# Optimization experiments

Measured on AMD Instinct MI355X. Metric: run time of the kernel, lower is better.

Reference implementation:

```python
import jax, jax.numpy as jnp
import numpy as np

M, B, S, D, H = 3, 32, 256, 768, 1024
LN_EPS = 1e-5


def _ln(x, g, b):
    m = jnp.mean(x, axis=-1, keepdims=True)
    v = jnp.mean((x - m) ** 2, axis=-1, keepdims=True)
    return (x - m) / jnp.sqrt(v + LN_EPS) * g + b


def setup_inputs() -> dict:
    key = jax.random.key(0)
    ks = jax.random.split(key, 16)
    sc = 0.02  # weight init scale
    return {
        "feats": jax.random.normal(ks[0], (M, B, S, D), jnp.float32),
        "Wq": jax.random.normal(ks[1], (M, D, D), jnp.float32) * sc,
        "bq": jnp.zeros((M, D), jnp.float32),
        "Wk": jax.random.normal(ks[2], (M, D, D), jnp.float32) * sc,
        "bk": jnp.zeros((M, D), jnp.float32),
        "Wv": jax.random.normal(ks[3], (M, D, D), jnp.float32) * sc,
        "bv": jnp.zeros((M, D), jnp.float32),
        "pgq_w": jax.random.normal(ks[4], (M, D), jnp.float32) * sc,
        "pgq_b": jnp.zeros((M,), jnp.float32),
        "pgk_w": jax.random.normal(ks[5], (M, D), jnp.float32) * sc,
        "pgk_b": jnp.zeros((M,), jnp.float32),
        "mu_w": jax.random.normal(ks[6], (M, D), jnp.float32) * sc,
        "mu_b": jnp.zeros((M,), jnp.float32),
        "lv_w": jax.random.normal(ks[7], (M, D), jnp.float32) * sc,
        "lv_b": jnp.zeros((M,), jnp.float32),
        "dyn": jnp.ones((1,), jnp.float32),
        "WE_w": jax.random.normal(ks[8], (M, D, D), jnp.float32) * sc,
        "WE_b": jnp.zeros((M, D), jnp.float32),
        "Wh_w": jax.random.normal(ks[9], (M, D, D), jnp.float32) * sc,
        "Wh_b": jnp.zeros((M, D), jnp.float32),
        "Wqc_w": jax.random.normal(ks[10], (M, D, D), jnp.float32) * sc,
        "Wqc_b": jnp.zeros((M, D), jnp.float32),
        "lnE_g": jnp.ones((M, D), jnp.float32),
        "lnE_b": jnp.zeros((M, D), jnp.float32),
        "lnG_g": jnp.ones((M, D), jnp.float32),
        "lnG_b": jnp.zeros((M, D), jnp.float32),
        "out_w": jax.random.normal(ks[11], (D * M, H), jnp.float32) * sc,
        "out_b": jnp.zeros((H,), jnp.float32),
        "eps": jax.random.normal(ks[12], (M, M - 1, B, S, 1), jnp.float32),
    }


def reference(feats, Wq, bq, Wk, bk, Wv, bv, pgq_w, pgq_b, pgk_w, pgk_b,
              mu_w, mu_b, lv_w, lv_b, dyn, WE_w, WE_b, Wh_w, Wh_b, Wqc_w, Wqc_b,
              lnE_g, lnE_b, lnG_g, lnG_b, out_w, out_b, eps):
    # batched per-modality projections: [M,B,S,D]
    Qs = jnp.einsum('mbsd,mde->mbse', feats, Wq) + bq[:, None, None, :]
    Ks = jnp.einsum('mbsd,mde->mbse', feats, Wk) + bk[:, None, None, :]
    Vs = jnp.einsum('mbsd,mde->mbse', feats, Wv) + bv[:, None, None, :]
    scale = 1.0 / jnp.sqrt(jnp.float32(D))

    kl = jnp.float32(0.0)
    outs = []
    for i in range(M):
        Qi = Qs[i]  # [B,S,D]
        mu = jnp.einsum('bsd,d->bs', Qi, mu_w[i])[..., None] + mu_b[i]      # [B,S,1]
        lv = jnp.einsum('bsd,d->bs', Qi, lv_w[i])[..., None] + lv_b[i]      # [B,S,1]
        std = jnp.exp(0.5 * lv)
        pq_base = jax.nn.sigmoid(
            jnp.einsum('bsd,d->bs', Qi, pgq_w[i])[..., None] + pgq_b[i])    # [B,S,1]
        kl_i = -0.5 * jnp.sum(1.0 + lv - mu ** 2 - jnp.exp(lv))
        agg = jnp.zeros_like(Qi)
        cnt = 0
        for j in range(M):
            if j == i:
                continue
            d_gate = mu + dyn * std * eps[i, cnt]  # reparameterization
            cnt += 1
            kl = kl + kl_i
            g = jax.nn.sigmoid(d_gate)             # [B,S,1]
            p_q = pq_base * g
            p_k = jax.nn.sigmoid(
                jnp.einsum('bsd,d->bs', Ks[j], pgk_w[i])[..., None] + pgk_b[i]) * g
            A = jnp.einsum('bqd,bkd->bqk', Qi, Ks[j]) * scale
            A = A * p_q * jnp.swapaxes(p_k, 1, 2)  # pregated scores
            W = jax.nn.softmax(A, axis=-1)
            agg = agg + jnp.einsum('bqk,bkd->bqd', W, Vs[j])
        # CAG
        E = jax.nn.relu(agg @ WE_w[i] + WE_b[i])
        G = jax.nn.relu(agg @ Wh_w[i] + Wh_b[i] + Qi @ Wqc_w[i] + Wqc_b[i])
        Ci = _ln(E, lnE_g[i], lnE_b[i]) * _ln(G, lnG_g[i], lnG_b[i])
        outs.append(Ci)
    fused = jnp.concatenate(outs, axis=-1)[:, 0, :]  # [B, M*D]
    out = fused @ out_w + out_b                       # [B, H]
    return out, kl
```

## Files before the change

kernel.cpp:

```cpp
#include <hip/hip_runtime.h>

#define M 3
#define B 32
#define S 256
#define D 768
#define H 1024
#define MD (M * D)
#define NP (M * (M - 1))
#define SCALE 0.03608439182435161f
#define LN_EPS 1e-5f

#define OFF_WMU   0
#define OFF_WLV   2304
#define OFF_WPGQ  4608
#define OFF_WPK   6912
#define OFF_CMU   11520
#define OFF_CLV   11523
#define OFF_CPGQ  11526
#define OFF_CPK   11529
#define OFF_MU    11552
#define OFF_LV    36128
#define OFF_PKPRE 60704
#define OFF_PQPRE 109856
#define OFF_Q     109952
// ... 12 lines not shown
    #pragma unroll
    for (int o = 32; o > 0; o >>= 1) v += __shfl_down(v, o, 64);
    return v;
}

__device__ __forceinline__ float sigmoidf(float x) {
    return 1.0f / (1.0f + __expf(-x));
}

__device__ __forceinline__ float dot4(float4 a, float4 b) {
    return a.x * b.x + a.y * b.y + a.z * b.z + a.w * b.w;
}

__device__ __forceinline__ void fma4(float4& a, float s, float4 w) {
    a.x += s * w.x; a.y += s * w.y; a.z += s * w.z; a.w += s * w.w;
}

__global__ __launch_bounds__(256) void k_prep(const float* Wq, const float* Wk,
        const float* bq, const float* bk,
        const float* mu_w, const float* mu_b, const float* lv_w, const float* lv_b,
        const float* pgq_w, const float* pgq_b, const float* pgk_w, const float* pgk_b,
        float* ws) {
    int blk = blockIdx.x;
    if (blk < 72) {
        int mat = blk / 12, rg = blk % 12;
        const float* Wm; const float *va, *vb, *vc;
        float *oa, *ob, *oc; int nv;
        if (mat < 3) {
            int i = mat;
            Wm = Wq + i * D * D;
            va = mu_w + i * D; vb = lv_w + i * D; vc = pgq_w + i * D;
            oa = ws + OFF_WMU + i * D; ob = ws + OFF_WLV + i * D; oc = ws + OFF_WPGQ + i * D;
            nv = 3;
        } else {
            int j = mat - 3;
            int i1 = (j == 0) ? 1 : 0, i2 = (j == 2) ? 1 : 2;
            int p1 = 2 * i1 + ((j < i1) ? j : j - 1);
            int p2 = 2 * i2 + ((j < i2) ? j : j - 1);
            Wm = Wk + j * D * D;
            va = pgk_w + i1 * D; vb = pgk_w + i2 * D; vc = va;
            oa = ws + OFF_WPK + p1 * D; ob = ws + OFF_WPK + p2 * D; oc = oa;
            nv = 2;
        }
        int wave = threadIdx.x >> 6, lane = threadIdx.x & 63;
        const float4* va4 = (const float4*)va;
        const float4* vb4 = (const float4*)vb;
// ... 39 lines not shown
        __shared__ float r[4];
        if ((t & 63) == 0) r[t >> 6] = part;
        __syncthreads();
        if (t == 0) *out = r[0] + r[1] + r[2] + r[3] + bias;
    } else {
        int r = blk - 87;
        int j = r / 144; r = r % 144;
        int d0 = (r / 12) * 64, e0 = (r % 12) * 64;
        __shared__ float tile[64][65];
        const float* src = Wk + j * D * D;
        for (int idx = threadIdx.x; idx < 4096; idx += 256) {
            int rr = idx / 64, cc = idx % 64;
            tile[rr][cc] = src[(d0 + rr) * D + e0 + cc];
        }
        __syncthreads();
        float* dst = ws + OFF_WKT + j * D * D;
        for (int idx = threadIdx.x; idx < 4096; idx += 256) {
            int rr = idx / 64, cc = idx % 64;
            dst[(e0 + rr) * D + d0 + cc] = tile[cc][rr];
        }
    }
}

__global__ __launch_bounds__(256) void k_stats(const float* feats, float* ws) {
    __shared__ float klred[4];
    int wave = threadIdx.x >> 6, lane = threadIdx.x & 63;
    int m = blockIdx.x / 512;
    int row0 = blockIdx.x * 16 + wave * 4;
    int i1 = (m == 0) ? 1 : 0, i2 = (m == 2) ? 1 : 2;
    int p0 = 2 * i1 + ((m < i1) ? m : m - 1);
    int p1 = 2 * i2 + ((m < i2) ? m : m - 1);
    const float4* wmu  = (const float4*)(ws + OFF_WMU + m * D);
    const float4* wlv  = (const float4*)(ws + OFF_WLV + m * D);
    const float4* wpgq = (const float4*)(ws + OFF_WPGQ + m * D);
    const float4* wpk0 = (const float4*)(ws + OFF_WPK + p0 * D);
    const float4* wpk1 = (const float4*)(ws + OFF_WPK + p1 * D);
    float4 U0 = wmu[lane],  U1 = wmu[lane + 64],  U2 = wmu[lane + 128];
    float4 L0 = wlv[lane],  L1 = wlv[lane + 64],  L2 = wlv[lane + 128];
    float4 Q0 = wpgq[lane], Q1 = wpgq[lane + 64], Q2 = wpgq[lane + 128];
    float4 P0 = wpk0[lane], P1 = wpk0[lane + 64], P2 = wpk0[lane + 128];
    float4 R0 = wpk1[lane], R1 = wpk1[lane + 64], R2 = wpk1[lane + 128];
    float4 x[4][3];
    #pragma unroll
    for (int rr = 0; rr < 4; rr++) {
        const float4* f = (const float4*)(feats + (size_t)(row0 + rr) * D);
        x[rr][0] = f[lane]; x[rr][1] = f[lane + 64]; x[rr][2] = f[lane + 128];
    }
    float amu[4], alv[4], apgq[4], apk0[4], apk1[4];
    #pragma unroll
    for (int rr = 0; rr < 4; rr++) {
        amu[rr]  = dot4(x[rr][0], U0) + dot4(x[rr][1], U1) + dot4(x[rr][2], U2);
        alv[rr]  = dot4(x[rr][0], L0) + dot4(x[rr][1], L1) + dot4(x[rr][2], L2);
        apgq[rr] = dot4(x[rr][0], Q0) + dot4(x[rr][1], Q1) + dot4(x[rr][2], Q2);
        apk0[rr] = dot4(x[rr][0], P0) + dot4(x[rr][1], P1) + dot4(x[rr][2], P2);
        apk1[rr] = dot4(x[rr][0], R0) + dot4(x[rr][1], R1) + dot4(x[rr][2], R2);
    }
    #pragma unroll
    for (int rr = 0; rr < 4; rr++) {
        amu[rr] = wave_reduce(amu[rr]);  alv[rr] = wave_reduce(alv[rr]);
        apgq[rr] = wave_reduce(apgq[rr]);
        apk0[rr] = wave_reduce(apk0[rr]); apk1[rr] = wave_reduce(apk1[rr]);
    }
    if (lane == 0) {
        float cmu = ws[OFF_CMU + m], clv = ws[OFF_CLV + m];
        float cpgq = ws[OFF_CPGQ + m];
        float cpk0 = ws[OFF_CPK + p0], cpk1 = ws[OFF_CPK + p1];
        float klsum = 0.f;
        #pragma unroll
        for (int rr = 0; rr < 4; rr++) {
            int row = row0 + rr;
            int rem = row % (B * S);
            int b = rem / S, s = rem % S;
            float muv = amu[rr] + cmu;
            float lvv = alv[rr] + clv;
            ws[OFF_MU + row] = muv;
            ws[OFF_LV + row] = lvv;
            ws[OFF_PKPRE + (p0 * B + b) * S + s] = apk0[rr] + cpk0;
            ws[OFF_PKPRE + (p1 * B + b) * S + s] = apk1[rr] + cpk1;
            if (s == 0) ws[OFF_PQPRE + m * B + b] = apgq[rr] + cpgq;
            klsum += 1.0f + lvv - muv * muv - __expf(lvv);
        }
        klred[wave] = klsum;
    }
    __syncthreads();
    if (threadIdx.x == 0)
        atomicAdd(ws + OFF_KL, -(klred[0] + klred[1] + klred[2] + klred[3]));
}


__global__ __launch_bounds__(192) void k_qrow(const float* feats, const float* Wq, float* ws) {
    int blk = blockIdx.x;
    int i = blk / 96, r = blk % 96, bg = r / 24, kc = r % 24;
    int kbase = kc * 32;
    __shared__ __align__(16) float xs[32][8];
    for (int idx = threadIdx.x; idx < 256; idx += 192) {
        int d = idx / 8, bb = idx % 8;
        xs[d][bb] = feats[((size_t)(i * B + bg * 8 + bb) * S) * D + kbase + d];
    }
    __syncthreads();
    int e4 = threadIdx.x * 4;
    const float* Wm = Wq + i * D * D + kbase * D + e4;
    float4 acc[8];
    #pragma unroll
    for (int bb = 0; bb < 8; bb++) acc[bb] = make_float4(0.f, 0.f, 0.f, 0.f);
    for (int k = 0; k < 32; k++) {
        float4 w = *(const float4*)(Wm + k * D);
        float4 x0 = *(const float4*)&xs[k][0];
        float4 x1 = *(const float4*)&xs[k][4];
        fma4(acc[0], x0.x, w); fma4(acc[1], x0.y, w);
        fma4(acc[2], x0.z, w); fma4(acc[3], x0.w, w);
        fma4(acc[4], x1.x, w); fma4(acc[5], x1.y, w);
        fma4(acc[6], x1.z, w); fma4(acc[7], x1.w, w);
    }
    #pragma unroll
    for (int bb = 0; bb < 8; bb++)
        *(float4*)&ws[OFF_ARENA + kc * 73728 + (i * 32 + bg * 8 + bb) * 768 + e4] = acc[bb];
}

__global__ __launch_bounds__(256) void k_red_q(const float* bq, const float* bk, float* ws) {
    int blk = blockIdx.x;
    int i = blk / B, b = blk % B;
    int fbase = (i * B + b) * D;
    int t = threadIdx.x;
    __shared__ float4 qsh[192];
    __shared__ float redsh[8];
    if (t < 192) {
        float4 a = *(const float4*)&bq[i * D + t * 4];
        #pragma unroll
        for (int kc = 0; kc < 24; kc++) {
            float4 v = *(const float4*)&ws[OFF_ARENA + kc * 73728 + fbase + t * 4];
            a.x += v.x; a.y += v.y; a.z += v.z; a.w += v.w;
        }
        *(float4*)&ws[OFF_Q + fbase + t * 4] = a;
        qsh[t] = a;
    }
    __syncthreads();
    int jA = (i == 0) ? 1 : 0, jB = (i == 2) ? 1 : 2;
    float pA_ = 0.f, pB_ = 0.f;
    if (t < 192) {
        float4 q = qsh[t];
        pA_ = dot4(q, *(const float4*)&bk[jA * D + t * 4]);
        pB_ = dot4(q, *(const float4*)&bk[jB * D + t * 4]);
    }
    pA_ = wave_reduce(pA_); pB_ = wave_reduce(pB_);
    int wave = t >> 6, lane = t & 63;
    if (lane == 0) { redsh[wave] = pA_; redsh[4 + wave] = pB_; }
    __syncthreads();
    if (t == 0) {
        ws[OFF_QBK + (2 * i) * B + b]     = redsh[0] + redsh[1] + redsh[2] + redsh[3];
        ws[OFF_QBK + (2 * i + 1) * B + b] = redsh[4] + redsh[5] + redsh[6] + redsh[7];
    }
}

__global__ __launch_bounds__(192) void k_qk(float* ws) {
    int blk = blockIdx.x;
    int j = blk / 96, r = blk % 96, vg = r / 12, kc = r % 12;
    int kbase = kc * 64;
    int i1 = (j == 0) ? 1 : 0, i2 = (j == 2) ? 1 : 2;
    __shared__ __align__(16) float xs[64][8];
    for (int idx = threadIdx.x; idx < 512; idx += 192) {
        int d = idx / 8, v = idx % 8;
        int v64 = vg * 8 + v;
        int i_ = (v64 < 32) ? i1 : i2, b = v64 & 31;
        xs[d][v] = ws[OFF_Q + (i_ * 32 + b) * 768 + kbase + d];
    }
    __syncthreads();
    int e4 = threadIdx.x * 4;
    const float* Wm = ws + OFF_WKT + j * D * D + kbase * D + e4;
    float4 acc[8];
    #pragma unroll
    for (int bb = 0; bb < 8; bb++) acc[bb] = make_float4(0.f, 0.f, 0.f, 0.f);
    for (int k = 0; k < 64; k++) {
        float4 w = *(const float4*)(Wm + k * D);
        float4 x0 = *(const float4*)&xs[k][0];
        float4 x1 = *(const float4*)&xs[k][4];
        fma4(acc[0], x0.x, w); fma4(acc[1], x0.y, w);
        fma4(acc[2], x0.z, w); fma4(acc[3], x0.w, w);
        fma4(acc[4], x1.x, w); fma4(acc[5], x1.y, w);
        fma4(acc[6], x1.z, w); fma4(acc[7], x1.w, w);
    }
    #pragma unroll
    for (int v = 0; v < 8; v++)
        *(float4*)&ws[OFF_ARENA + kc * 147456 + (j * 64 + vg * 8 + v) * 768 + e4] = acc[v];
}

__global__ __launch_bounds__(256) void k_red_qk(float* ws) {
    int idx = blockIdx.x * 256 + threadIdx.x;
    int fidx = idx * 4;
    int p = fidx / 24576, rem = fidx % 24576;
    int b = rem / 768, d = rem % 768;
    int i = p / 2, c = p % 2, j = c + (c >= i ? 1 : 0);
    int i1 = (j == 0) ? 1 : 0;
    int iidx = (i == i1) ? 0 : 1;
    int vg = iidx * 32 + b;
    float4 a = make_float4(0.f, 0.f, 0.f, 0.f);
    #pragma unroll
    for (int kc = 0; kc < 12; kc++) {
        float4 pp = *(const float4*)&ws[OFF_ARENA + kc * 147456 + (j * 64 + vg) * 768 + d];
        a.x += pp.x; a.y += pp.y; a.z += pp.z; a.w += pp.w;
    }
    *(float4*)&ws[OFF_QK + fidx] = a;
}

__global__ __launch_bounds__(256) void k_score(const float* feats, float* ws) {
    int blk = blockIdx.x;
    int j = blk / 128, r = blk % 128, b = r / 4, kc = r % 4;
    int i1 = (j == 0) ? 1 : 0, i2 = (j == 2) ? 1 : 2;
    int pA = 2 * i1 + ((j < i1) ? j : j - 1);
    int pB = 2 * i2 + ((j < i2) ? j : j - 1);
    int wave = threadIdx.x >> 6, lane = threadIdx.x & 63;
    const float4* qa4 = (const float4*)(ws + OFF_QK + (pA * B + b) * D);
    const float4* qb4 = (const float4*)(ws + OFF_QK + (pB * B + b) * D);
    float4 qA0 = qa4[lane], qA1 = qa4[lane + 64], qA2 = qa4[lane + 128];
    float4 qB0 = qb4[lane], qB1 = qb4[lane + 64], qB2 = qb4[lane + 128];
    const float* fbase = feats + ((j * B + b) * S) * D;
    float* scA = ws + OFF_ARENA + ((j * B + b) * 2) * S;
    float* scB = scA + S;
    int k0 = kc * 64 + wave * 16;
    for (int k = k0; k < k0 + 16; k += 4) {
        float4 x[4][3];
        #pragma unroll
        for (int rr = 0; rr < 4; rr++) {
            const float4* f = (const float4*)(fbase + (k + rr) * D);
            x[rr][0] = f[lane]; x[rr][1] = f[lane + 64]; x[rr][2] = f[lane + 128];
        }
        float dA[4], dB[4];
        #pragma unroll
        for (int rr = 0; rr < 4; rr++) {
            dA[rr] = dot4(x[rr][0], qA0) + dot4(x[rr][1], qA1) + dot4(x[rr][2], qA2);
            dB[rr] = dot4(x[rr][0], qB0) + dot4(x[rr][1], qB1) + dot4(x[rr][2], qB2);
        }
        #pragma unroll
        for (int rr = 0; rr < 4; rr++) { dA[rr] = wave_reduce(dA[rr]); dB[rr] = wave_reduce(dB[rr]); }
        if (lane == 0) {
            #pragma unroll
            for (int rr = 0; rr < 4; rr++) { scA[k + rr] = dA[rr]; scB[k + rr] = dB[rr]; }
        }
    }
}

__global__ __launch_bounds__(256) void k_wsum(const float* feats, const float* eps,
                                              const float* dyn, float* ws) {
    int blk = blockIdx.x;
    int j = blk / 96, r = blk % 96, b = r / 3, dc = r % 3;
    int i1 = (j == 0) ? 1 : 0, i2 = (j == 2) ? 1 : 2;
    int pA = 2 * i1 + ((j < i1) ? j : j - 1);
    int pB = 2 * i2 + ((j < i2) ? j : j - 1);
    __shared__ float sA[S], sB[S], redm[256];
    int t = threadIdx.x;
    float dynv = dyn[0];
    const float* rawA = ws + OFF_ARENA + ((j * B + b) * 2) * S;
    const float* rawB = rawA + S;
    {
        float muk = ws[OFF_MU + (i1 * B + b) * S + t];
        float lvk = ws[OFF_LV + (i1 * B + b) * S + t];
        float ek  = eps[(pA * B + b) * S + t];
        float g   = sigmoidf(muk + dynv * __expf(0.5f * lvk) * ek);
        float pk  = sigmoidf(ws[OFF_PKPRE + (pA * B + b) * S + t]) * g;
        float mu0 = ws[OFF_MU + (i1 * B + b) * S];
        float lv0 = ws[OFF_LV + (i1 * B + b) * S];
        float e0  = eps[(pA * B + b) * S];
// ... 28 lines not shown
    for (int st = 128; st > 0; st >>= 1) { if (t < st) redm[t] = fmaxf(redm[t], redm[t + st]); __syncthreads(); }
    float mxB = redm[0]; __syncthreads();
    float wB = __expf(sB[t] - mxB);
    redm[t] = wB; __syncthreads();
    for (int st = 128; st > 0; st >>= 1) { if (t < st) redm[t] += redm[t + st]; __syncthreads(); }
    float sumB = redm[0]; __syncthreads();
    sB[t] = wB / sumB;
    __syncthreads();
    int dim = dc * 256 + t;
    const float* fcol = feats + ((j * B + b) * S) * D + dim;
    float accA = 0.f, accB = 0.f;
    #pragma unroll 8
    for (int k = 0; k < S; k++) {
        float fv = fcol[k * D];
        accA += sA[k] * fv;
        accB += sB[k] * fv;
    }
    ws[OFF_FSUM + (pA * B + b) * D + dim] = accA;
    ws[OFF_FSUM + (pB * B + b) * D + dim] = accB;
}

__global__ __launch_bounds__(192) void k_agg(const float* Wv, float* ws) {
    int blk = blockIdx.x;
    int i = blk / 96, r = blk % 96, bg = r / 24, kc = r % 24;
    int kbase = kc * 32;
    int j0 = (i == 0) ? 1 : 0, j1 = (i == 2) ? 1 : 2;
    int p0 = 2 * i, p1 = 2 * i + 1;
    __shared__ __align__(16) float xs0[32][8], xs1[32][8];
    for (int idx = threadIdx.x; idx < 256; idx += 192) {
        int d = idx / 8, bb = idx % 8;
        xs0[d][bb] = ws[OFF_FSUM + (p0 * B + bg * 8 + bb) * D + kbase + d];
        xs1[d][bb] = ws[OFF_FSUM + (p1 * B + bg * 8 + bb) * D + kbase + d];
    }
    __syncthreads();
    int e4 = threadIdx.x * 4;
    const float* W0 = Wv + j0 * D * D + kbase * D + e4;
    const float* W1 = Wv + j1 * D * D + kbase * D + e4;
    float4 acc[8];
    #pragma unroll
    for (int bb = 0; bb < 8; bb++) acc[bb] = make_float4(0.f, 0.f, 0.f, 0.f);
    for (int k = 0; k < 32; k++) {
        float4 w0 = *(const float4*)(W0 + k * D);
        float4 w1 = *(const float4*)(W1 + k * D);
        float4 a0 = *(const float4*)&xs0[k][0];
        float4 a1 = *(const float4*)&xs0[k][4];
        float4 b0 = *(const float4*)&xs1[k][0];
        float4 b1 = *(const float4*)&xs1[k][4];
        fma4(acc[0], a0.x, w0); fma4(acc[1], a0.y, w0);
        fma4(acc[2], a0.z, w0); fma4(acc[3], a0.w, w0);
        fma4(acc[4], a1.x, w0); fma4(acc[5], a1.y, w0);
        fma4(acc[6], a1.z, w0); fma4(acc[7], a1.w, w0);
        fma4(acc[0], b0.x, w1); fma4(acc[1], b0.y, w1);
        fma4(acc[2], b0.z, w1); fma4(acc[3], b0.w, w1);
        fma4(acc[4], b1.x, w1); fma4(acc[5], b1.y, w1);
        fma4(acc[6], b1.z, w1); fma4(acc[7], b1.w, w1);
    }
    #pragma unroll
    for (int bb = 0; bb < 8; bb++)
        *(float4*)&ws[OFF_ARENA + kc * 73728 + (i * 32 + bg * 8 + bb) * 768 + e4] = acc[bb];
}

__global__ __launch_bounds__(256) void k_red_agg(const float* bv, float* ws) {
    int idx = blockIdx.x * 256 + threadIdx.x;
    int fidx = idx * 4;
    int i = fidx / 24576, e = fidx % 768;
    int j0 = (i == 0) ? 1 : 0, j1 = (i == 2) ? 1 : 2;
    float4 b0 = *(const float4*)&bv[j0 * 768 + e];
    float4 b1 = *(const float4*)&bv[j1 * 768 + e];
    float4 a = make_float4(b0.x + b1.x, b0.y + b1.y, b0.z + b1.z, b0.w + b1.w);
    const float* base = ws + OFF_ARENA;
    #pragma unroll
    for (int kc = 0; kc < 24; kc++) {
        float4 p = *(const float4*)&base[kc * 73728 + fidx];
        a.x += p.x; a.y += p.y; a.z += p.z; a.w += p.w;
    }
    *(float4*)&ws[OFF_AGG + fidx] = a;
}

__global__ __launch_bounds__(192) void k_eg(const float* WE_w, const float* Wh_w,
                                            const float* Wqc_w, float* ws) {
    int blk = blockIdx.x;
    int kind = blk / 144, r = blk % 144;
    int i = r / 48, r2 = r % 48, bg = r2 / 12, kc = r2 % 12;
    int kbase = kc * 64;
    __shared__ __align__(16) float xa[64][8], xq[64][8];
    for (int idx = threadIdx.x; idx < 512; idx += 192) {
        int d = idx / 8, bb = idx % 8;
        xa[d][bb] = ws[OFF_AGG + (i * B + bg * 8 + bb) * D + kbase + d];
        if (kind) xq[d][bb] = ws[OFF_Q + (i * B + bg * 8 + bb) * D + kbase + d];
    }
    __syncthreads();
    int e4 = threadIdx.x * 4;
    float4 acc[8];
    #pragma unroll
    for (int bb = 0; bb < 8; bb++) acc[bb] = make_float4(0.f, 0.f, 0.f, 0.f);
    if (kind == 0) {
        const float* Wm = WE_w + i * D * D + kbase * D + e4;
        for (int k = 0; k < 64; k++) {
            float4 w = *(const float4*)(Wm + k * D);
            float4 a0 = *(const float4*)&xa[k][0];
            float4 a1 = *(const float4*)&xa[k][4];
            fma4(acc[0], a0.x, w); fma4(acc[1], a0.y, w);
            fma4(acc[2], a0.z, w); fma4(acc[3], a0.w, w);
            fma4(acc[4], a1.x, w); fma4(acc[5], a1.y, w);
            fma4(acc[6], a1.z, w); fma4(acc[7], a1.w, w);
        }
    } else {
        const float* Wh = Wh_w + i * D * D + kbase * D + e4;
        const float* Wc = Wqc_w + i * D * D + kbase * D + e4;
        for (int k = 0; k < 64; k++) {
            float4 wh = *(const float4*)(Wh + k * D);
            float4 wc = *(const float4*)(Wc + k * D);
            float4 a0 = *(const float4*)&xa[k][0];
            float4 a1 = *(const float4*)&xa[k][4];
            float4 q0 = *(const float4*)&xq[k][0];
            float4 q1 = *(const float4*)&xq[k][4];
            fma4(acc[0], a0.x, wh); fma4(acc[1], a0.y, wh);
            fma4(acc[2], a0.z, wh); fma4(acc[3], a0.w, wh);
            fma4(acc[4], a1.x, wh); fma4(acc[5], a1.y, wh);
            fma4(acc[6], a1.z, wh); fma4(acc[7], a1.w, wh);
            fma4(acc[0], q0.x, wc); fma4(acc[1], q0.y, wc);
            fma4(acc[2], q0.z, wc); fma4(acc[3], q0.w, wc);
            fma4(acc[4], q1.x, wc); fma4(acc[5], q1.y, wc);
            fma4(acc[6], q1.z, wc); fma4(acc[7], q1.w, wc);
        }
    }
    int base = OFF_ARENA + (kind ? 884736 : 0) + kc * 73728;
    #pragma unroll
    for (int bb = 0; bb < 8; bb++)
        *(float4*)&ws[base + (i * 32 + bg * 8 + bb) * 768 + e4] = acc[bb];
}

__global__ __launch_bounds__(256) void k_red_eg(const float* WE_b, const float* Wh_b,
                                                const float* Wqc_b, float* ws) {
    int blk = blockIdx.x;
    bool isG = blk >= 72;
    int idx = (isG ? blk - 72 : blk) * 256 + threadIdx.x;
    int fidx = idx * 4;
    int i = fidx / 24576, e = fidx % 768;
    float4 a;
    const float* base = ws + OFF_ARENA + (isG ? 884736 : 0);
    if (isG) {
        float4 b0 = *(const float4*)&Wh_b[i * 768 + e];
        float4 b1 = *(const float4*)&Wqc_b[i * 768 + e];
        a = make_float4(b0.x + b1.x, b0.y + b1.y, b0.z + b1.z, b0.w + b1.w);
    } else {
        a = *(const float4*)&WE_b[i * 768 + e];
    }
    #pragma unroll
    for (int kc = 0; kc < 12; kc++) {
        float4 p = *(const float4*)&base[kc * 73728 + fidx];
        a.x += p.x; a.y += p.y; a.z += p.z; a.w += p.w;
    }
// ... 15 lines not shown
    r2[t] = e0 * e0 + e1 * e1 + e2 * e2;
    r3[t] = g0 + g1 + g2;
    r4[t] = g0 * g0 + g1 * g1 + g2 * g2;
    __syncthreads();
    for (int st = 128; st > 0; st >>= 1) {
        if (t < st) { r1[t] += r1[t + st]; r2[t] += r2[t + st]; r3[t] += r3[t + st]; r4[t] += r4[t + st]; }
        __syncthreads();
    }
    float mE = r1[0] * (1.0f / D), vE = r2[0] * (1.0f / D) - mE * mE;
    float mG = r3[0] * (1.0f / D), vG = r4[0] * (1.0f / D) - mG * mG;
    float sE = rsqrtf(vE + LN_EPS), sG = rsqrtf(vG + LN_EPS);
    float* o = ws + OFF_FUSED + b * MD + i * D;
    const float* eg = lnE_g + i * D; const float* ebv = lnE_b + i * D;
    const float* gg = lnG_g + i * D; const float* gbv = lnG_b + i * D;
    o[t]       = ((e0 - mE) * sE * eg[t]       + ebv[t])       * ((g0 - mG) * sG * gg[t]       + gbv[t]);
    o[t + 256] = ((e1 - mE) * sE * eg[t + 256] + ebv[t + 256]) * ((g1 - mG) * sG * gg[t + 256] + gbv[t + 256]);
    o[t + 512] = ((e2 - mE) * sE * eg[t + 512] + ebv[t + 512]) * ((g2 - mG) * sG * gg[t + 512] + gbv[t + 512]);
}

__global__ __launch_bounds__(256) void k_out(const float* out_w, float* ws) {
    int blk = blockIdx.x;
    int bg = blk / 36, kc = blk % 36;
    int kbase = kc * 64;
    __shared__ __align__(16) float xs[64][8];
    for (int idx = threadIdx.x; idx < 512; idx += 256) {
        int d = idx / 8, bb = idx % 8;
        xs[d][bb] = ws[OFF_FUSED + (bg * 8 + bb) * MD + kbase + d];
    }
    __syncthreads();
    int e4 = threadIdx.x * 4;
    const float* Wm = out_w + kbase * H + e4;
    float4 acc[8];
    #pragma unroll
    for (int bb = 0; bb < 8; bb++) acc[bb] = make_float4(0.f, 0.f, 0.f, 0.f);
    for (int k = 0; k < 64; k++) {
        float4 w = *(const float4*)(Wm + k * H);
        float4 x0 = *(const float4*)&xs[k][0];
        float4 x1 = *(const float4*)&xs[k][4];
        fma4(acc[0], x0.x, w); fma4(acc[1], x0.y, w);
        fma4(acc[2], x0.z, w); fma4(acc[3], x0.w, w);
        fma4(acc[4], x1.x, w); fma4(acc[5], x1.y, w);
        fma4(acc[6], x1.z, w); fma4(acc[7], x1.w, w);
    }
    #pragma unroll
    for (int bb = 0; bb < 8; bb++)
        *(float4*)&ws[OFF_ARENA + kc * 32768 + (bg * 8 + bb) * 1024 + e4] = acc[bb];
}

__global__ __launch_bounds__(256) void k_fin(const float* out_b, float* ws, float* out) {
    int b = blockIdx.x;
    int h4 = threadIdx.x * 4;
    float4 a = *(const float4*)&out_b[h4];
    #pragma unroll
    for (int kc = 0; kc < 36; kc++) {
        float4 p = *(const float4*)&ws[OFF_ARENA + kc * 32768 + b * 1024 + h4];
        a.x += p.x; a.y += p.y; a.z += p.z; a.w += p.w;
    }
    *(float4*)&out[b * H + h4] = a;
    if (b == 0 && threadIdx.x == 0) out[B * H] = ws[OFF_KL];
}

extern "C" void kernel_launch(void* const* d_in, const int* in_sizes, int n_in,
                              void* d_out, int out_size, void* d_ws, size_t ws_size,
                              hipStream_t stream) {
    const float* feats = (const float*)d_in[0];
    const float* Wq    = (const float*)d_in[1];
    const float* bq    = (const float*)d_in[2];
    const float* Wk    = (const float*)d_in[3];
    const float* bk    = (const float*)d_in[4];
// ... 4 lines not shown
    const float* pgk_w = (const float*)d_in[9];
    const float* pgk_b = (const float*)d_in[10];
    const float* mu_w  = (const float*)d_in[11];
    const float* mu_b  = (const float*)d_in[12];
    const float* lv_w  = (const float*)d_in[13];
    const float* lv_b  = (const float*)d_in[14];
    const float* dyn   = (const float*)d_in[15];
    const float* WE_w  = (const float*)d_in[16];
    const float* WE_b  = (const float*)d_in[17];
    const float* Wh_w  = (const float*)d_in[18];
    const float* Wh_b  = (const float*)d_in[19];
    const float* Wqc_w = (const float*)d_in[20];
    const float* Wqc_b = (const float*)d_in[21];
    const float* lnE_g = (const float*)d_in[22];
    const float* lnE_b = (const float*)d_in[23];
    const float* lnG_g = (const float*)d_in[24];
    const float* lnG_b = (const float*)d_in[25];
    const float* out_w = (const float*)d_in[26];
    const float* out_b = (const float*)d_in[27];
    const float* eps   = (const float*)d_in[28];
    float* ws  = (float*)d_ws;
    float* out = (float*)d_out;

    hipMemsetAsync((char*)d_ws + OFF_KL * sizeof(float), 0, sizeof(float), stream);

    k_prep<<<519, 256, 0, stream>>>(Wq, Wk, bq, bk, mu_w, mu_b, lv_w, lv_b,
                                    pgq_w, pgq_b, pgk_w, pgk_b, ws);
    k_stats<<<1536, 256, 0, stream>>>(feats, ws);
    k_qrow<<<288, 192, 0, stream>>>(feats, Wq, ws);
    k_red_q<<<96, 256, 0, stream>>>(bq, bk, ws);
    k_qk<<<288, 192, 0, stream>>>(ws);
    k_red_qk<<<144, 256, 0, stream>>>(ws);
    k_score<<<384, 256, 0, stream>>>(feats, ws);
    k_wsum<<<288, 256, 0, stream>>>(feats, eps, dyn, ws);
    k_agg<<<288, 192, 0, stream>>>(Wv, ws);
    k_red_agg<<<72, 256, 0, stream>>>(bv, ws);
    k_eg<<<288, 192, 0, stream>>>(WE_w, Wh_w, Wqc_w, ws);
    k_red_eg<<<144, 256, 0, stream>>>(WE_b, Wh_b, Wqc_b, ws);
    k_ln<<<M * B, 256, 0, stream>>>(lnE_g, lnE_b, lnG_g, lnG_b, ws);
    k_out<<<144, 256, 0, stream>>>(out_w, ws);
    k_fin<<<32, 256, 0, stream>>>(out_b, ws, out);
}
```

Measured before the change: 360.9 us.

## Fuse per-row gate statistics into score kernel and widen batch tiles to 16

Removes the separate k_stats pass over all of feats by computing the mu, logvar and p_k projections, the KL partial sums and the pq prelogit inside k_score, which already streams the same feature rows. The KL accumulator is now zeroed inside k_prep, replacing the separate memset. The skinny GEMM kernels (qrow, qk, agg, eg, out) now process 16 batch rows per block instead of 8, halving grid sizes and doubling weight reuse per load. The trade-off is more registers per thread and fewer blocks, which may leave CUs idle. k_score also now issues many more wave reductions per row.

After: 417.1 us. 15.6% more time.

```diff
diff --git a/kernel.cpp b/kernel.cpp
--- a/kernel.cpp
+++ b/kernel.cpp
@@ -58,6 +58,7 @@
         const float* pgq_w, const float* pgq_b, const float* pgk_w, const float* pgk_b,
         float* ws) {
     int blk = blockIdx.x;
+    if (blk == 0 && threadIdx.x == 0) ws[OFF_KL] = 0.f;
     if (blk < 72) {
         int mat = blk / 12, rg = blk % 12;
         const float* Wm; const float *va, *vb, *vc;
@@ -143,99 +144,39 @@
     }
 }
 
-__global__ __launch_bounds__(256) void k_stats(const float* feats, float* ws) {
-    __shared__ float klred[4];
-    int wave = threadIdx.x >> 6, lane = threadIdx.x & 63;
-    int m = blockIdx.x / 512;
-    int row0 = blockIdx.x * 16 + wave * 4;
-    int i1 = (m == 0) ? 1 : 0, i2 = (m == 2) ? 1 : 2;
-    int p0 = 2 * i1 + ((m < i1) ? m : m - 1);
-    int p1 = 2 * i2 + ((m < i2) ? m : m - 1);
-    const float4* wmu  = (const float4*)(ws + OFF_WMU + m * D);
-    const float4* wlv  = (const float4*)(ws + OFF_WLV + m * D);
-    const float4* wpgq = (const float4*)(ws + OFF_WPGQ + m * D);
-    const float4* wpk0 = (const float4*)(ws + OFF_WPK + p0 * D);
-    const float4* wpk1 = (const float4*)(ws + OFF_WPK + p1 * D);
-    float4 U0 = wmu[lane],  U1 = wmu[lane + 64],  U2 = wmu[lane + 128];
-    float4 L0 = wlv[lane],  L1 = wlv[lane + 64],  L2 = wlv[lane + 128];
-    float4 Q0 = wpgq[lane], Q1 = wpgq[lane + 64], Q2 = wpgq[lane + 128];
-    float4 P0 = wpk0[lane], P1 = wpk0[lane + 64], P2 = wpk0[lane + 128];
-    float4 R0 = wpk1[lane], R1 = wpk1[lane + 64], R2 = wpk1[lane + 128];
-    float4 x[4][3];
-    #pragma unroll
-    for (int rr = 0; rr < 4; rr++) {
-        const float4* f = (const float4*)(feats + (size_t)(row0 + rr) * D);
-        x[rr][0] = f[lane]; x[rr][1] = f[lane + 64]; x[rr][2] = f[lane + 128];
-    }
-    float amu[4], alv[4], apgq[4], apk0[4], apk1[4];
-    #pragma unroll
-    for (int rr = 0; rr < 4; rr++) {
-        amu[rr]  = dot4(x[rr][0], U0) + dot4(x[rr][1], U1) + dot4(x[rr][2], U2);
-        alv[rr]  = dot4(x[rr][0], L0) + dot4(x[rr][1], L1) + dot4(x[rr][2], L2);
-        apgq[rr] = dot4(x[rr][0], Q0) + dot4(x[rr][1], Q1) + dot4(x[rr][2], Q2);
-        apk0[rr] = dot4(x[rr][0], P0) + dot4(x[rr][1], P1) + dot4(x[rr][2], P2);
-        apk1[rr] = dot4(x[rr][0], R0) + dot4(x[rr][1], R1) + dot4(x[rr][2], R2);
-    }
-    #pragma unroll
-    for (int rr = 0; rr < 4; rr++) {
-        amu[rr] = wave_reduce(amu[rr]);  alv[rr] = wave_reduce(alv[rr]);
-        apgq[rr] = wave_reduce(apgq[rr]);
-        apk0[rr] = wave_reduce(apk0[rr]); apk1[rr] = wave_reduce(apk1[rr]);
-    }
-    if (lane == 0) {
-        float cmu = ws[OFF_CMU + m], clv = ws[OFF_CLV + m];
-        float cpgq = ws[OFF_CPGQ + m];
-        float cpk0 = ws[OFF_CPK + p0], cpk1 = ws[OFF_CPK + p1];
-        float klsum = 0.f;
-        #pragma unroll
-        for (int rr = 0; rr < 4; rr++) {
-            int row = row0 + rr;
-            int rem = row % (B * S);
-            int b = rem / S, s = rem % S;
-            float muv = amu[rr] + cmu;
-            float lvv = alv[rr] + clv;
-            ws[OFF_MU + row] = muv;
-            ws[OFF_LV + row] = lvv;
-            ws[OFF_PKPRE + (p0 * B + b) * S + s] = apk0[rr] + cpk0;
-            ws[OFF_PKPRE + (p1 * B + b) * S + s] = apk1[rr] + cpk1;
-            if (s == 0) ws[OFF_PQPRE + m * B + b] = apgq[rr] + cpgq;
-            klsum += 1.0f + lvv - muv * muv - __expf(lvv);
-        }
-        klred[wave] = klsum;
-    }
-    __syncthreads();
-    if (threadIdx.x == 0)
-        atomicAdd(ws + OFF_KL, -(klred[0] + klred[1] + klred[2] + klred[3]));
-}
-
-
 __global__ __launch_bounds__(192) void k_qrow(const float* feats, const float* Wq, float* ws) {
     int blk = blockIdx.x;
-    int i = blk / 96, r = blk % 96, bg = r / 24, kc = r % 24;
+    int i = blk / 48, r = blk % 48, bg = r / 24, kc = r % 24;
     int kbase = kc * 32;
-    __shared__ __align__(16) float xs[32][8];
-    for (int idx = threadIdx.x; idx < 256; idx += 192) {
-        int d = idx / 8, bb = idx % 8;
-        xs[d][bb] = feats[((size_t)(i * B + bg * 8 + bb) * S) * D + kbase + d];
+    __shared__ __align__(16) float xs[32][16];
+    for (int idx = threadIdx.x; idx < 512; idx += 192) {
+        int d = idx / 16, bb = idx % 16;
+        xs[d][bb] = feats[((size_t)(i * B + bg * 16 + bb) * S) * D + kbase + d];
     }
     __syncthreads();
     int e4 = threadIdx.x * 4;
     const float* Wm = Wq + i * D * D + kbase * D + e4;
-    float4 acc[8];
-    #pragma unroll
-    for (int bb = 0; bb < 8; bb++) acc[bb] = make_float4(0.f, 0.f, 0.f, 0.f);
+    float4 acc[16];
+    #pragma unroll
+    for (int bb = 0; bb < 16; bb++) acc[bb] = make_float4(0.f, 0.f, 0.f, 0.f);
     for (int k = 0; k < 32; k++) {
         float4 w = *(const float4*)(Wm + k * D);
         float4 x0 = *(const float4*)&xs[k][0];
         float4 x1 = *(const float4*)&xs[k][4];
-        fma4(acc[0], x0.x, w); fma4(acc[1], x0.y, w);
-        fma4(acc[2], x0.z, w); fma4(acc[3], x0.w, w);
-        fma4(acc[4], x1.x, w); fma4(acc[5], x1.y, w);
-        fma4(acc[6], x1.z, w); fma4(acc[7], x1.w, w);
-    }
-    #pragma unroll
-    for (int bb = 0; bb < 8; bb++)
-        *(float4*)&ws[OFF_ARENA + kc * 73728 + (i * 32 + bg * 8 + bb) * 768 + e4] = acc[bb];
+        float4 x2 = *(const float4*)&xs[k][8];
+        float4 x3 = *(const float4*)&xs[k][12];
+        fma4(acc[0], x0.x, w);  fma4(acc[1], x0.y, w);
+        fma4(acc[2], x0.z, w);  fma4(acc[3], x0.w, w);
+        fma4(acc[4], x1.x, w);  fma4(acc[5], x1.y, w);
+        fma4(acc[6], x1.z, w);  fma4(acc[7], x1.w, w);
+        fma4(acc[8], x2.x, w);  fma4(acc[9], x2.y, w);
+        fma4(acc[10], x2.z, w); fma4(acc[11], x2.w, w);
+        fma4(acc[12], x3.x, w); fma4(acc[13], x3.y, w);
+        fma4(acc[14], x3.z, w); fma4(acc[15], x3.w, w);
+    }
+    #pragma unroll
+    for (int bb = 0; bb < 16; bb++)
+        *(float4*)&ws[OFF_ARENA + kc * 73728 + (i * 32 + bg * 16 + bb) * 768 + e4] = acc[bb];
 }
 
 __global__ __launch_bounds__(256) void k_red_q(const float* bq, const float* bk, float* ws) {
@@ -275,34 +216,40 @@
 
 __global__ __launch_bounds__(192) void k_qk(float* ws) {
     int blk = blockIdx.x;
-    int j = blk / 96, r = blk % 96, vg = r / 12, kc = r % 12;
+    int j = blk / 48, r = blk % 48, vg = r / 12, kc = r % 12;
     int kbase = kc * 64;
     int i1 = (j == 0) ? 1 : 0, i2 = (j == 2) ? 1 : 2;
-    __shared__ __align__(16) float xs[64][8];
-    for (int idx = threadIdx.x; idx < 512; idx += 192) {
-        int d = idx / 8, v = idx % 8;
-        int v64 = vg * 8 + v;
+    __shared__ __align__(16) float xs[64][16];
+    for (int idx = threadIdx.x; idx < 1024; idx += 192) {
+        int d = idx / 16, v = idx % 16;
+        int v64 = vg * 16 + v;
         int i_ = (v64 < 32) ? i1 : i2, b = v64 & 31;
         xs[d][v] = ws[OFF_Q + (i_ * 32 + b) * 768 + kbase + d];
     }
     __syncthreads();
     int e4 = threadIdx.x * 4;
     const float* Wm = ws + OFF_WKT + j * D * D + kbase * D + e4;
-    float4 acc[8];
-    #pragma unroll
-    for (int bb = 0; bb < 8; bb++) acc[bb] = make_float4(0.f, 0.f, 0.f, 0.f);
+    float4 acc[16];
+    #pragma unroll
+    for (int bb = 0; bb < 16; bb++) acc[bb] = make_float4(0.f, 0.f, 0.f, 0.f);
     for (int k = 0; k < 64; k++) {
         float4 w = *(const float4*)(Wm + k * D);
         float4 x0 = *(const float4*)&xs[k][0];
         float4 x1 = *(const float4*)&xs[k][4];
-        fma4(acc[0], x0.x, w); fma4(acc[1], x0.y, w);
-        fma4(acc[2], x0.z, w); fma4(acc[3], x0.w, w);
-        fma4(acc[4], x1.x, w); fma4(acc[5], x1.y, w);
-        fma4(acc[6], x1.z, w); fma4(acc[7], x1.w, w);
-    }
-    #pragma unroll
-    for (int v = 0; v < 8; v++)
-        *(float4*)&ws[OFF_ARENA + kc * 147456 + (j * 64 + vg * 8 + v) * 768 + e4] = acc[v];
+        float4 x2 = *(const float4*)&xs[k][8];
+        float4 x3 = *(const float4*)&xs[k][12];
+        fma4(acc[0], x0.x, w);  fma4(acc[1], x0.y, w);
+        fma4(acc[2], x0.z, w);  fma4(acc[3], x0.w, w);
+        fma4(acc[4], x1.x, w);  fma4(acc[5], x1.y, w);
+        fma4(acc[6], x1.z, w);  fma4(acc[7], x1.w, w);
+        fma4(acc[8], x2.x, w);  fma4(acc[9], x2.y, w);
+        fma4(acc[10], x2.z, w); fma4(acc[11], x2.w, w);
+        fma4(acc[12], x3.x, w); fma4(acc[13], x3.y, w);
+        fma4(acc[14], x3.z, w); fma4(acc[15], x3.w, w);
+    }
+    #pragma unroll
+    for (int v = 0; v < 16; v++)
+        *(float4*)&ws[OFF_ARENA + kc * 147456 + (j * 64 + vg * 16 + v) * 768 + e4] = acc[v];
 }
 
 __global__ __launch_bounds__(256) void k_red_qk(float* ws) {
@@ -334,30 +281,67 @@
     const float4* qb4 = (const float4*)(ws + OFF_QK + (pB * B + b) * D);
     float4 qA0 = qa4[lane], qA1 = qa4[lane + 64], qA2 = qa4[lane + 128];
     float4 qB0 = qb4[lane], qB1 = qb4[lane + 64], qB2 = qb4[lane + 128];
-    const float* fbase = feats + ((j * B + b) * S) * D;
+    const float4* wmu4 = (const float4*)(ws + OFF_WMU + j * D);
+    const float4* wlv4 = (const float4*)(ws + OFF_WLV + j * D);
+    const float4* wk04 = (const float4*)(ws + OFF_WPK + pA * D);
+    const float4* wk14 = (const float4*)(ws + OFF_WPK + pB * D);
+    float4 U0 = wmu4[lane], U1 = wmu4[lane + 64], U2 = wmu4[lane + 128];
+    float4 L0 = wlv4[lane], L1 = wlv4[lane + 64], L2 = wlv4[lane + 128];
+    float4 K00 = wk04[lane], K01 = wk04[lane + 64], K02 = wk04[lane + 128];
+    float4 K10 = wk14[lane], K11 = wk14[lane + 64], K12 = wk14[lane + 128];
+    const float* fb = feats + ((j * B + b) * S) * D;
     float* scA = ws + OFF_ARENA + ((j * B + b) * 2) * S;
     float* scB = scA + S;
+    float cmu = ws[OFF_CMU + j], clv = ws[OFF_CLV + j];
+    float cpk0 = ws[OFF_CPK + pA], cpk1 = ws[OFF_CPK + pB];
+    if (kc == 0 && wave == 0) {
+        const float4* wg4 = (const float4*)(ws + OFF_WPGQ + j * D);
+        const float4* f0 = (const float4*)fb;
+        float dd = dot4(f0[lane], wg4[lane]) + dot4(f0[lane + 64], wg4[lane + 64])
+                 + dot4(f0[lane + 128], wg4[lane + 128]);
+        dd = wave_reduce(dd);
+        if (lane == 0) ws[OFF_PQPRE + j * B + b] = dd + ws[OFF_CPGQ + j];
+    }
     int k0 = kc * 64 + wave * 16;
-    for (int k = k0; k < k0 + 16; k += 4) {
-        float4 x[4][3];
-        #pragma unroll
-        for (int rr = 0; rr < 4; rr++) {
-            const float4* f = (const float4*)(fbase + (k + rr) * D);
-            x[rr][0] = f[lane]; x[rr][1] = f[lane + 64]; x[rr][2] = f[lane + 128];
-        }
-        float dA[4], dB[4];
-        #pragma unroll
-        for (int rr = 0; rr < 4; rr++) {
-            dA[rr] = dot4(x[rr][0], qA0) + dot4(x[rr][1], qA1) + dot4(x[rr][2], qA2);
-            dB[rr] = dot4(x[rr][0], qB0) + dot4(x[rr][1], qB1) + dot4(x[rr][2], qB2);
-        }
-        #pragma unroll
-        for (int rr = 0; rr < 4; rr++) { dA[rr] = wave_reduce(dA[rr]); dB[rr] = wave_reduce(dB[rr]); }
+    float klsum = 0.f;
+    for (int k = k0; k < k0 + 16; k += 2) {
+        const float4* fA = (const float4*)(fb + k * D);
+        const float4* fB = (const float4*)(fb + (k + 1) * D);
+        float4 a0 = fA[lane], a1 = fA[lane + 64], a2 = fA[lane + 128];
+        float4 b0 = fB[lane], b1 = fB[lane + 64], b2 = fB[lane + 128];
+        float sa1 = dot4(a0, qA0) + dot4(a1, qA1) + dot4(a2, qA2);
+        float sb1 = dot4(a0, qB0) + dot4(a1, qB1) + dot4(a2, qB2);
+        float mu1 = dot4(a0, U0) + dot4(a1, U1) + dot4(a2, U2);
+        float lv1 = dot4(a0, L0) + dot4(a1, L1) + dot4(a2, L2);
+        float p01 = dot4(a0, K00) + dot4(a1, K01) + dot4(a2, K02);
+        float p11 = dot4(a0, K10) + dot4(a1, K11) + dot4(a2, K12);
+        float sa2 = dot4(b0, qA0) + dot4(b1, qA1) + dot4(b2, qA2);
+        float sb2 = dot4(b0, qB0) + dot4(b1, qB1) + dot4(b2, qB2);
+        float mu2 = dot4(b0, U0) + dot4(b1, U1) + dot4(b2, U2);
+        float lv2 = dot4(b0, L0) + dot4(b1, L1) + dot4(b2, L2);
+        float p02 = dot4(b0, K00) + dot4(b1, K01) + dot4(b2, K02);
+        float p12 = dot4(b0, K10) + dot4(b1, K11) + dot4(b2, K12);
+        sa1 = wave_reduce(sa1); sb1 = wave_reduce(sb1);
+        mu1 = wave_reduce(mu1); lv1 = wave_reduce(lv1);
+        p01 = wave_reduce(p01); p11 = wave_reduce(p11);
+        sa2 = wave_reduce(sa2); sb2 = wave_reduce(sb2);
+        mu2 = wave_reduce(mu2); lv2 = wave_reduce(lv2);
+        p02 = wave_reduce(p02); p12 = wave_reduce(p12);
         if (lane == 0) {
-            #pragma unroll
-            for (int rr = 0; rr < 4; rr++) { scA[k + rr] = dA[rr]; scB[k + rr] = dB[rr]; }
-        }
-    }
+            scA[k] = sa1; scB[k] = sb1; scA[k + 1] = sa2; scB[k + 1] = sb2;
+            float m1 = mu1 + cmu, l1 = lv1 + clv;
+            float m2 = mu2 + cmu, l2 = lv2 + clv;
+            int row = (j * B + b) * S + k;
+            ws[OFF_MU + row] = m1;      ws[OFF_MU + row + 1] = m2;
+            ws[OFF_LV + row] = l1;      ws[OFF_LV + row + 1] = l2;
+            ws[OFF_PKPRE + (pA * B + b) * S + k]     = p01 + cpk0;
+            ws[OFF_PKPRE + (pA * B + b) * S + k + 1] = p02 + cpk0;
+            ws[OFF_PKPRE + (pB * B + b) * S + k]     = p11 + cpk1;
+            ws[OFF_PKPRE + (pB * B + b) * S + k + 1] = p12 + cpk1;
+            klsum += 2.0f + l1 + l2 - m1 * m1 - m2 * m2 - __expf(l1) - __expf(l2);
+        }
+    }
+    if (lane == 0) atomicAdd(ws + OFF_KL, -klsum);
 }
 
 __global__ __launch_bounds__(256) void k_wsum(const float* feats, const float* eps,
@@ -432,42 +416,54 @@
 
 __global__ __launch_bounds__(192) void k_agg(const float* Wv, float* ws) {
     int blk = blockIdx.x;
-    int i = blk / 96, r = blk % 96, bg = r / 24, kc = r % 24;
+    int i = blk / 48, r = blk % 48, bg = r / 24, kc = r % 24;
     int kbase = kc * 32;
     int j0 = (i == 0) ? 1 : 0, j1 = (i == 2) ? 1 : 2;
     int p0 = 2 * i, p1 = 2 * i + 1;
-    __shared__ __align__(16) float xs0[32][8], xs1[32][8];
-    for (int idx = threadIdx.x; idx < 256; idx += 192) {
-        int d = idx / 8, bb = idx % 8;
-        xs0[d][bb] = ws[OFF_FSUM + (p0 * B + bg * 8 + bb) * D + kbase + d];
-        xs1[d][bb] = ws[OFF_FSUM + (p1 * B + bg * 8 + bb) * D + kbase + d];
+    __shared__ __align__(16) float xs0[32][16], xs1[32][16];
+    for (int idx = threadIdx.x; idx < 512; idx += 192) {
+        int d = idx / 16, bb = idx % 16;
+        xs0[d][bb] = ws[OFF_FSUM + (p0 * B + bg * 16 + bb) * D + kbase + d];
+        xs1[d][bb] = ws[OFF_FSUM + (p1 * B + bg * 16 + bb) * D + kbase + d];
     }
     __syncthreads();
     int e4 = threadIdx.x * 4;
     const float* W0 = Wv + j0 * D * D + kbase * D + e4;
     const float* W1 = Wv + j1 * D * D + kbase * D + e4;
-    float4 acc[8];
-    #pragma unroll
-    for (int bb = 0; bb < 8; bb++) acc[bb] = make_float4(0.f, 0.f, 0.f, 0.f);
+    float4 acc[16];
+    #pragma unroll
+    for (int bb = 0; bb < 16; bb++) acc[bb] = make_float4(0.f, 0.f, 0.f, 0.f);
     for (int k = 0; k < 32; k++) {
         float4 w0 = *(const float4*)(W0 + k * D);
         float4 w1 = *(const float4*)(W1 + k * D);
         float4 a0 = *(const float4*)&xs0[k][0];
         float4 a1 = *(const float4*)&xs0[k][4];
-        float4 b0 = *(const float4*)&xs1[k][0];
-        float4 b1 = *(const float4*)&xs1[k][4];
-        fma4(acc[0], a0.x, w0); fma4(acc[1], a0.y, w0);
-        fma4(acc[2], a0.z, w0); fma4(acc[3], a0.w, w0);
-        fma4(acc[4], a1.x, w0); fma4(acc[5], a1.y, w0);
-        fma4(acc[6], a1.z, w0); fma4(acc[7], a1.w, w0);
-        fma4(acc[0], b0.x, w1); fma4(acc[1], b0.y, w1);
-        fma4(acc[2], b0.z, w1); fma4(acc[3], b0.w, w1);
-        fma4(acc[4], b1.x, w1); fma4(acc[5], b1.y, w1);
-        fma4(acc[6], b1.z, w1); fma4(acc[7], b1.w, w1);
-    }
-    #pragma unroll
-    for (int bb = 0; bb < 8; bb++)
-        *(float4*)&ws[OFF_ARENA + kc * 73728 + (i * 32 + bg * 8 + bb) * 768 + e4] = acc[bb];
+        float4 a2 = *(const float4*)&xs0[k][8];
+        float4 a3 = *(const float4*)&xs0[k][12];
+        float4 c0 = *(const float4*)&xs1[k][0];
+        float4 c1 = *(const float4*)&xs1[k][4];
+        float4 c2 = *(const float4*)&xs1[k][8];
+        float4 c3 = *(const float4*)&xs1[k][12];
+        fma4(acc[0], a0.x, w0);  fma4(acc[1], a0.y, w0);
+        fma4(acc[2], a0.z, w0);  fma4(acc[3], a0.w, w0);
+        fma4(acc[4], a1.x, w0);  fma4(acc[5], a1.y, w0);
+        fma4(acc[6], a1.z, w0);  fma4(acc[7], a1.w, w0);
+        fma4(acc[8], a2.x, w0);  fma4(acc[9], a2.y, w0);
+        fma4(acc[10], a2.z, w0); fma4(acc[11], a2.w, w0);
+        fma4(acc[12], a3.x, w0); fma4(acc[13], a3.y, w0);
+        fma4(acc[14], a3.z, w0); fma4(acc[15], a3.w, w0);
+        fma4(acc[0], c0.x, w1);  fma4(acc[1], c0.y, w1);
+        fma4(acc[2], c0.z, w1);  fma4(acc[3], c0.w, w1);
+        fma4(acc[4], c1.x, w1);  fma4(acc[5], c1.y, w1);
+        fma4(acc[6], c1.z, w1);  fma4(acc[7], c1.w, w1);
+        fma4(acc[8], c2.x, w1);  fma4(acc[9], c2.y, w1);
+        fma4(acc[10], c2.z, w1); fma4(acc[11], c2.w, w1);
+        fma4(acc[12], c3.x, w1); fma4(acc[13], c3.y, w1);
+        fma4(acc[14], c3.z, w1); fma4(acc[15], c3.w, w1);
+    }
+    #pragma unroll
+    for (int bb = 0; bb < 16; bb++)
+        *(float4*)&ws[OFF_ARENA + kc * 73728 + (i * 32 + bg * 16 + bb) * 768 + e4] = acc[bb];
 }
 
 __global__ __launch_bounds__(256) void k_red_agg(const float* bv, float* ws) {
@@ -490,30 +486,36 @@
 __global__ __launch_bounds__(192) void k_eg(const float* WE_w, const float* Wh_w,
                                             const float* Wqc_w, float* ws) {
     int blk = blockIdx.x;
-    int kind = blk / 144, r = blk % 144;
-    int i = r / 48, r2 = r % 48, bg = r2 / 12, kc = r2 % 12;
+    int kind = blk / 72, r = blk % 72;
+    int i = r / 24, r2 = r % 24, bg = r2 / 12, kc = r2 % 12;
     int kbase = kc * 64;
-    __shared__ __align__(16) float xa[64][8], xq[64][8];
-    for (int idx = threadIdx.x; idx < 512; idx += 192) {
-        int d = idx / 8, bb = idx % 8;
-        xa[d][bb] = ws[OFF_AGG + (i * B + bg * 8 + bb) * D + kbase + d];
-        if (kind) xq[d][bb] = ws[OFF_Q + (i * B + bg * 8 + bb) * D + kbase + d];
+    __shared__ __align__(16) float xa[64][16], xq[64][16];
+    for (int idx = threadIdx.x; idx < 1024; idx += 192) {
+        int d = idx / 16, bb = idx % 16;
+        xa[d][bb] = ws[OFF_AGG + (i * B + bg * 16 + bb) * D + kbase + d];
+        if (kind) xq[d][bb] = ws[OFF_Q + (i * B + bg * 16 + bb) * D + kbase + d];
     }
     __syncthreads();
     int e4 = threadIdx.x * 4;
-    float4 acc[8];
-    #pragma unroll
-    for (int bb = 0; bb < 8; bb++) acc[bb] = make_float4(0.f, 0.f, 0.f, 0.f);
+    float4 acc[16];
+    #pragma unroll
+    for (int bb = 0; bb < 16; bb++) acc[bb] = make_float4(0.f, 0.f, 0.f, 0.f);
     if (kind == 0) {
         const float* Wm = WE_w + i * D * D + kbase * D + e4;
         for (int k = 0; k < 64; k++) {
             float4 w = *(const float4*)(Wm + k * D);
             float4 a0 = *(const float4*)&xa[k][0];
             float4 a1 = *(const float4*)&xa[k][4];
-            fma4(acc[0], a0.x, w); fma4(acc[1], a0.y, w);
-            fma4(acc[2], a0.z, w); fma4(acc[3], a0.w, w);
-            fma4(acc[4], a1.x, w); fma4(acc[5], a1.y, w);
-            fma4(acc[6], a1.z, w); fma4(acc[7], a1.w, w);
+            float4 a2 = *(const float4*)&xa[k][8];
+            float4 a3 = *(const float4*)&xa[k][12];
+            fma4(acc[0], a0.x, w);  fma4(acc[1], a0.y, w);
+            fma4(acc[2], a0.z, w);  fma4(acc[3], a0.w, w);
+            fma4(acc[4], a1.x, w);  fma4(acc[5], a1.y, w);
+            fma4(acc[6], a1.z, w);  fma4(acc[7], a1.w, w);
+            fma4(acc[8], a2.x, w);  fma4(acc[9], a2.y, w);
+            fma4(acc[10], a2.z, w); fma4(acc[11], a2.w, w);
+            fma4(acc[12], a3.x, w); fma4(acc[13], a3.y, w);
+            fma4(acc[14], a3.z, w); fma4(acc[15], a3.w, w);
         }
     } else {
         const float* Wh = Wh_w + i * D * D + kbase * D + e4;
@@ -523,22 +525,34 @@
             float4 wc = *(const float4*)(Wc + k * D);
             float4 a0 = *(const float4*)&xa[k][0];
             float4 a1 = *(const float4*)&xa[k][4];
+            float4 a2 = *(const float4*)&xa[k][8];
+            float4 a3 = *(const float4*)&xa[k][12];
             float4 q0 = *(const float4*)&xq[k][0];
             float4 q1 = *(const float4*)&xq[k][4];
-            fma4(acc[0], a0.x, wh); fma4(acc[1], a0.y, wh);
-            fma4(acc[2], a0.z, wh); fma4(acc[3], a0.w, wh);
-            fma4(acc[4], a1.x, wh); fma4(acc[5], a1.y, wh);
-            fma4(acc[6], a1.z, wh); fma4(acc[7], a1.w, wh);
-            fma4(acc[0], q0.x, wc); fma4(acc[1], q0.y, wc);
-            fma4(acc[2], q0.z, wc); fma4(acc[3], q0.w, wc);
-            fma4(acc[4], q1.x, wc); fma4(acc[5], q1.y, wc);
-            fma4(acc[6], q1.z, wc); fma4(acc[7], q1.w, wc);
+            float4 q2 = *(const float4*)&xq[k][8];
+            float4 q3 = *(const float4*)&xq[k][12];
+            fma4(acc[0], a0.x, wh);  fma4(acc[1], a0.y, wh);
+            fma4(acc[2], a0.z, wh);  fma4(acc[3], a0.w, wh);
+            fma4(acc[4], a1.x, wh);  fma4(acc[5], a1.y, wh);
+            fma4(acc[6], a1.z, wh);  fma4(acc[7], a1.w, wh);
+            fma4(acc[8], a2.x, wh);  fma4(acc[9], a2.y, wh);
+            fma4(acc[10], a2.z, wh); fma4(acc[11], a2.w, wh);
+            fma4(acc[12], a3.x, wh); fma4(acc[13], a3.y, wh);
+            fma4(acc[14], a3.z, wh); fma4(acc[15], a3.w, wh);
+            fma4(acc[0], q0.x, wc);  fma4(acc[1], q0.y, wc);
+            fma4(acc[2], q0.z, wc);  fma4(acc[3], q0.w, wc);
+            fma4(acc[4], q1.x, wc);  fma4(acc[5], q1.y, wc);
+            fma4(acc[6], q1.z, wc);  fma4(acc[7], q1.w, wc);
+            fma4(acc[8], q2.x, wc);  fma4(acc[9], q2.y, wc);
+            fma4(acc[10], q2.z, wc); fma4(acc[11], q2.w, wc);
+            fma4(acc[12], q3.x, wc); fma4(acc[13], q3.y, wc);
+            fma4(acc[14], q3.z, wc); fma4(acc[15], q3.w, wc);
         }
     }
     int base = OFF_ARENA + (kind ? 884736 : 0) + kc * 73728;
     #pragma unroll
-    for (int bb = 0; bb < 8; bb++)
-        *(float4*)&ws[base + (i * 32 + bg * 8 + bb) * 768 + e4] = acc[bb];
+    for (int bb = 0; bb < 16; bb++)
+        *(float4*)&ws[base + (i * 32 + bg * 16 + bb) * 768 + e4] = acc[bb];
 }
 
 __global__ __launch_bounds__(256) void k_red_eg(const float* WE_b, const float* Wh_b,
@@ -600,29 +614,35 @@
     int blk = blockIdx.x;
     int bg = blk / 36, kc = blk % 36;
     int kbase = kc * 64;
-    __shared__ __align__(16) float xs[64][8];
-    for (int idx = threadIdx.x; idx < 512; idx += 256) {
-        int d = idx / 8, bb = idx % 8;
-        xs[d][bb] = ws[OFF_FUSED + (bg * 8 + bb) * MD + kbase + d];
+    __shared__ __align__(16) float xs[64][16];
+    for (int idx = threadIdx.x; idx < 1024; idx += 256) {
+        int d = idx / 16, bb = idx % 16;
+        xs[d][bb] = ws[OFF_FUSED + (bg * 16 + bb) * MD + kbase + d];
     }
     __syncthreads();
     int e4 = threadIdx.x * 4;
     const float* Wm = out_w + kbase * H + e4;
-    float4 acc[8];
-    #pragma unroll
-    for (int bb = 0; bb < 8; bb++) acc[bb] = make_float4(0.f, 0.f, 0.f, 0.f);
+    float4 acc[16];
+    #pragma unroll
+    for (int bb = 0; bb < 16; bb++) acc[bb] = make_float4(0.f, 0.f, 0.f, 0.f);
     for (int k = 0; k < 64; k++) {
         float4 w = *(const float4*)(Wm + k * H);
         float4 x0 = *(const float4*)&xs[k][0];
         float4 x1 = *(const float4*)&xs[k][4];
-        fma4(acc[0], x0.x, w); fma4(acc[1], x0.y, w);
-        fma4(acc[2], x0.z, w); fma4(acc[3], x0.w, w);
-        fma4(acc[4], x1.x, w); fma4(acc[5], x1.y, w);
-        fma4(acc[6], x1.z, w); fma4(acc[7], x1.w, w);
-    }
-    #pragma unroll
-    for (int bb = 0; bb < 8; bb++)
-        *(float4*)&ws[OFF_ARENA + kc * 32768 + (bg * 8 + bb) * 1024 + e4] = acc[bb];
+        float4 x2 = *(const float4*)&xs[k][8];
+        float4 x3 = *(const float4*)&xs[k][12];
+        fma4(acc[0], x0.x, w);  fma4(acc[1], x0.y, w);
+        fma4(acc[2], x0.z, w);  fma4(acc[3], x0.w, w);
+        fma4(acc[4], x1.x, w);  fma4(acc[5], x1.y, w);
+        fma4(acc[6], x1.z, w);  fma4(acc[7], x1.w, w);
+        fma4(acc[8], x2.x, w);  fma4(acc[9], x2.y, w);
+        fma4(acc[10], x2.z, w); fma4(acc[11], x2.w, w);
+        fma4(acc[12], x3.x, w); fma4(acc[13], x3.y, w);
+        fma4(acc[14], x3.z, w); fma4(acc[15], x3.w, w);
+    }
+    #pragma unroll
+    for (int bb = 0; bb < 16; bb++)
+        *(float4*)&ws[OFF_ARENA + kc * 32768 + (bg * 16 + bb) * 1024 + e4] = acc[bb];
 }
 
 __global__ __launch_bounds__(256) void k_fin(const float* out_b, float* ws, float* out) {
@@ -673,22 +693,19 @@
     float* ws  = (float*)d_ws;
     float* out = (float*)d_out;
 
-    hipMemsetAsync((char*)d_ws + OFF_KL * sizeof(float), 0, sizeof(float), stream);
-
     k_prep<<<519, 256, 0, stream>>>(Wq, Wk, bq, bk, mu_w, mu_b, lv_w, lv_b,
                                     pgq_w, pgq_b, pgk_w, pgk_b, ws);
-    k_stats<<<1536, 256, 0, stream>>>(feats, ws);
-    k_qrow<<<288, 192, 0, stream>>>(feats, Wq, ws);
+    k_qrow<<<144, 192, 0, stream>>>(feats, Wq, ws);
     k_red_q<<<96, 256, 0, stream>>>(bq, bk, ws);
-    k_qk<<<288, 192, 0, stream>>>(ws);
+    k_qk<<<144, 192, 0, stream>>>(ws);
     k_red_qk<<<144, 256, 0, stream>>>(ws);
     k_score<<<384, 256, 0, stream>>>(feats, ws);
     k_wsum<<<288, 256, 0, stream>>>(feats, eps, dyn, ws);
-    k_agg<<<288, 192, 0, stream>>>(Wv, ws);
+    k_agg<<<144, 192, 0, stream>>>(Wv, ws);
     k_red_agg<<<72, 256, 0, stream>>>(bv, ws);
-    k_eg<<<288, 192, 0, stream>>>(WE_w, Wh_w, Wqc_w, ws);
+    k_eg<<<144, 192, 0, stream>>>(WE_w, Wh_w, Wqc_w, ws);
     k_red_eg<<<144, 256, 0, stream>>>(WE_b, Wh_b, Wqc_b, ws);
     k_ln<<<M * B, 256, 0, stream>>>(lnE_g, lnE_b, lnG_g, lnG_b, ws);
-    k_out<<<144, 256, 0, stream>>>(out_w, ws);
+    k_out<<<72, 256, 0, stream>>>(out_w, ws);
     k_fin<<<32, 256, 0, stream>>>(out_b, ws, out);
 }
```
